# Kernel optimization log

Measured on AMD Instinct MI355X. Metric: run time of the kernel, lower is better.

Reference implementation:

```python
import jax, jax.numpy as jnp
import numpy as np
from jax import lax

B, T, F = 128, 100, 64
HID = [16, 32]  # encoder hidden dims; decoder uses reversed [32, 16]
K = 3


def _conv2d(x, w, b):
    # x: [N, Cin, H, W], w: [Cout, Cin, kh, kw] -> 'SAME' padding as in torch padding=k//2
    y = lax.conv_general_dilated(x, w, (1, 1), 'SAME',
                                 dimension_numbers=('NCHW', 'OIHW', 'NCHW'))
    return y + b[None, :, None, None]


def _convlstm_layer(xs, w, b, h0, c0):
    # xs: [T, B, Cin, H, W] time-major; returns hidden seq [T,B,Chid,H,W] and final (h, c)
    def step(carry, x_t):
        h, c = carry
        z = _conv2d(jnp.concatenate([x_t, h], axis=1), w, b)
        i, f, o, g = jnp.split(z, 4, axis=1)  # gate order i, f, o, g
        c2 = jax.nn.sigmoid(f) * c + jax.nn.sigmoid(i) * jnp.tanh(g)
        h2 = jax.nn.sigmoid(o) * jnp.tanh(c2)
        return (h2, c2), h2
    (hT, cT), hs = lax.scan(step, (h0, c0), xs)
    return hs, (hT, cT)


def setup_inputs() -> dict:
    key = jax.random.key(0)
    ks = jax.random.split(key, 12)
    s = 0.05
    inp = {
        'x': jax.random.normal(ks[0], (B, T, F), dtype=jnp.float32),
        # encoder layer 0: in=1+16, out=4*16
        'enc_w0': jax.random.normal(ks[1], (4 * HID[0], 1 + HID[0], K, K), dtype=jnp.float32) * s,
        'enc_b0': jnp.zeros((4 * HID[0],), dtype=jnp.float32),
        # encoder layer 1: in=16+32, out=4*32
        'enc_w1': jax.random.normal(ks[2], (4 * HID[1], HID[0] + HID[1], K, K), dtype=jnp.float32) * s,
        'enc_b1': jnp.zeros((4 * HID[1],), dtype=jnp.float32),
        # decoder layer 0: hidden=32, input=32 (last encoder hidden)
        'dec_w0': jax.random.normal(ks[3], (4 * HID[1], HID[1] + HID[1], K, K), dtype=jnp.float32) * s,
        'dec_b0': jnp.zeros((4 * HID[1],), dtype=jnp.float32),
        # decoder layer 1: hidden=16, input=32
        'dec_w1': jax.random.normal(ks[4], (4 * HID[0], HID[1] + HID[0], K, K), dtype=jnp.float32) * s,
        'dec_b1': jnp.zeros((4 * HID[0],), dtype=jnp.float32),
        # final 1x1 conv: 16 -> 1
        'fc_w': jax.random.normal(ks[5], (1, HID[0], 1, 1), dtype=jnp.float32) * s,
        'fc_b': jnp.zeros((1,), dtype=jnp.float32),
    }
    return inp


def reference(x, enc_w0, enc_b0, enc_w1, enc_b1, dec_w0, dec_b0, dec_w1, dec_b1, fc_w, fc_b):
    b, t, f = x.shape
    # [b,t,f] -> [t,b,1,f,1] time-major, spatial (f,1)
    xs = jnp.transpose(x.reshape(b, t, 1, f, 1), (1, 0, 2, 3, 4))
    z16 = jnp.zeros((b, HID[0], f, 1), x.dtype)
    z32 = jnp.zeros((b, HID[1], f, 1), x.dtype)

    enc1, (h1, c1) = _convlstm_layer(xs, enc_w0, enc_b0, z16, z16)
    enc2, (h2, c2) = _convlstm_layer(enc1, enc_w1, enc_b1, z32, z32)

    # decoder initial states = encoder final states reversed
    dec1, _ = _convlstm_layer(enc2, dec_w0, dec_b0, h2, c2)
    dec2, _ = _convlstm_layer(dec1, dec_w1, dec_b1, h1, c1)  # [t,b,16,f,1]

    # final 1x1 conv applied per timestep == one batched conv over t*b
    flat = dec2.reshape(t * b, HID[0], f, 1)
    out = _conv2d(flat, fc_w, fc_b)  # [t*b,1,f,1]
    recon = jnp.transpose(out.reshape(t, b, f), (1, 0, 2))  # [b,t,f]
    return recon
```

## Files before the change

kernel.cpp:

```cpp
#include <hip/hip_runtime.h>
#include <math.h>

#define B_ 128
#define T_ 100
#define RS 72
#define RS2 40

__device__ __forceinline__ float frcp_(float x){ return __builtin_amdgcn_rcpf(x); }
__device__ __forceinline__ float fsig_(float x){ return frcp_(1.f + __expf(-x)); }
__device__ __forceinline__ float ftanh_(float x){ float e = __expf(2.f*x); return 1.f - 2.f*frcp_(e+1.f); }
__device__ __forceinline__ float gate1(float zi, float zf, float zo, float zg, float& c){
    float cc = fsig_(zf)*c + fsig_(zi)*ftanh_(zg);
    c = cc;
    return fsig_(zo)*ftanh_(cc);
}
__device__ __forceinline__ float4 ldf4(const float* p){ return *reinterpret_cast<const float4*>(p); }
__device__ __forceinline__ void stf4(float* p, float4 v){ *reinterpret_cast<float4*>(p) = v; }
__device__ __forceinline__ float2 ldf2(const float* p){ return *reinterpret_cast<const float2*>(p); }
__device__ __forceinline__ void stf2(float* p, float2 v){ *reinterpret_cast<float2*>(p) = v; }
__device__ __forceinline__ float4 add4(float4 a, float4 b){
    return make_float4(a.x+b.x, a.y+b.y, a.z+b.z, a.w+b.w);
}
__device__ __forceinline__ float4 gate4(float4 zi, float4 zf, float4 zo, float4 zg,
                                        float bi, float bf, float bo, float bg, float4& c){
    float4 h;
    h.x = gate1(zi.x+bi, zf.x+bf, zo.x+bo, zg.x+bg, c.x);
    h.y = gate1(zi.y+bi, zf.y+bf, zo.y+bo, zg.y+bg, c.y);
    h.z = gate1(zi.z+bi, zf.z+bf, zo.z+bo, zg.z+bg, c.z);
    h.w = gate1(zi.w+bi, zf.w+bf, zo.w+bo, zg.w+bg, c.w);
    return h;
}

__device__ __forceinline__ void fma4v(float w, float u0,float u1,float u2,float u3, float4& a){
    a.x = fmaf(w,u0,a.x); a.y = fmaf(w,u1,a.y);
    a.z = fmaf(w,u2,a.z); a.w = fmaf(w,u3,a.w);
}
__device__ __forceinline__ void fma2v(float w, float u0,float u1, float2& a){
    a.x = fmaf(w,u0,a.x); a.y = fmaf(w,u1,a.y);
}

template<int ROWS>
__device__ __forceinline__ void rowacc4(const float* __restrict__ rowp,
                                        const float* __restrict__ wk,
                                        float4& ai, float4& af, float4& ao, float4& ag)
{
    float  m = rowp[-1];
    float4 a = ldf4(rowp);
    float  p = rowp[4];
    float4 wa = ldf4(wk);
    float4 wb = ldf4(wk + ROWS);
    float4 wc = ldf4(wk + 2*ROWS);
    fma4v(wa.x, m,a.x,a.y,a.z, ai);  fma4v(wa.y, m,a.x,a.y,a.z, af);
    fma4v(wa.z, m,a.x,a.y,a.z, ao);  fma4v(wa.w, m,a.x,a.y,a.z, ag);
    fma4v(wb.x, a.x,a.y,a.z,a.w, ai); fma4v(wb.y, a.x,a.y,a.z,a.w, af);
    fma4v(wb.z, a.x,a.y,a.z,a.w, ao); fma4v(wb.w, a.x,a.y,a.z,a.w, ag);
    fma4v(wc.x, a.y,a.z,a.w,p, ai);  fma4v(wc.y, a.y,a.z,a.w,p, af);
    fma4v(wc.z, a.y,a.z,a.w,p, ao);  fma4v(wc.w, a.y,a.z,a.w,p, ag);
}
template<int ROWS>
__device__ __forceinline__ void rowacc2(const float* __restrict__ rowp,
                                        const float* __restrict__ wk,
                                        float2& ai, float2& af, float2& ao, float2& ag)
{
    float  m = rowp[-1];
    float2 a = *reinterpret_cast<const float2*>(rowp);
    float  p = rowp[2];
    float4 wa = ldf4(wk);
    float4 wb = ldf4(wk + ROWS);
    float4 wc = ldf4(wk + 2*ROWS);
    fma2v(wa.x, m,a.x, ai); fma2v(wa.y, m,a.x, af);
    fma2v(wa.z, m,a.x, ao); fma2v(wa.w, m,a.x, ag);
    fma2v(wb.x, a.x,a.y, ai); fma2v(wb.y, a.x,a.y, af);
    fma2v(wb.z, a.x,a.y, ao); fma2v(wb.w, a.x,a.y, ag);
    fma2v(wc.x, a.y,p, ai); fma2v(wc.y, a.y,p, af);
    fma2v(wc.z, a.y,p, ao); fma2v(wc.w, a.y,p, ag);
}
template<int ROWS>
__device__ __forceinline__ void rowacc8(const float* __restrict__ rowp,
                                        const float* __restrict__ wk,
                                        float4& i0, float4& i1, float4& f0v, float4& f1v,
                                        float4& o0, float4& o1, float4& g0, float4& g1)
{
    float  m = rowp[-1];
    float4 a = ldf4(rowp);
    float4 b = ldf4(rowp + 4);
    float  p = rowp[8];
    float4 wa = ldf4(wk);
    float4 wb = ldf4(wk + ROWS);
    float4 wc = ldf4(wk + 2*ROWS);
    fma4v(wa.x, m,a.x,a.y,a.z, i0);   fma4v(wa.x, a.w,b.x,b.y,b.z, i1);
    fma4v(wa.y, m,a.x,a.y,a.z, f0v);  fma4v(wa.y, a.w,b.x,b.y,b.z, f1v);
    fma4v(wa.z, m,a.x,a.y,a.z, o0);   fma4v(wa.z, a.w,b.x,b.y,b.z, o1);
    fma4v(wa.w, m,a.x,a.y,a.z, g0);   fma4v(wa.w, a.w,b.x,b.y,b.z, g1);
    fma4v(wb.x, a.x,a.y,a.z,a.w, i0); fma4v(wb.x, b.x,b.y,b.z,b.w, i1);
    fma4v(wb.y, a.x,a.y,a.z,a.w, f0v);fma4v(wb.y, b.x,b.y,b.z,b.w, f1v);
    fma4v(wb.z, a.x,a.y,a.z,a.w, o0); fma4v(wb.z, b.x,b.y,b.z,b.w, o1);
    fma4v(wb.w, a.x,a.y,a.z,a.w, g0); fma4v(wb.w, b.x,b.y,b.z,b.w, g1);
    fma4v(wc.x, a.y,a.z,a.w,b.x, i0); fma4v(wc.x, b.y,b.z,b.w,p, i1);
    fma4v(wc.y, a.y,a.z,a.w,b.x, f0v);fma4v(wc.y, b.y,b.z,b.w,p, f1v);
    fma4v(wc.z, a.y,a.z,a.w,b.x, o0); fma4v(wc.z, b.y,b.z,b.w,p, o1);
    fma4v(wc.w, a.y,a.z,a.w,b.x, g0); fma4v(wc.w, b.y,b.z,b.w,p, g1);
}

__global__ __launch_bounds__(512, 1) void enc_kernel(
    const float* __restrict__ x,
    const float* __restrict__ w0, const float* __restrict__ b0,
    const float* __restrict__ w1, const float* __restrict__ b1,
    float* __restrict__ seq,
    float* __restrict__ h1f, float* __restrict__ c1f,
    float* __restrict__ h2f, float* __restrict__ c2f,
    float* __restrict__ comm, int* __restrict__ flags)
{
    __shared__ float wl0[51 * 64];
    __shared__ float wl1[144 * 128];
    __shared__ float bs0[64];
    __shared__ float bs1[128];
    __shared__ float hbuf[50 * RS2];
    __shared__ float zsA[4 * 16 * 32];
    __shared__ float zsB[4 * 32 * 32];

    const int tid = threadIdx.x;
    const int b = blockIdx.x & 127;
    const int s = blockIdx.x >> 7;
    const int gofs = s << 5;
    const int kg = tid >> 8;
    const int r  = tid & 255;
    const int chB = r >> 3, f0B = (r & 7) * 4;
    const int chA = r >> 4, f0A = (r & 15) * 2;
    const int haloSlot = s ? 3 : 36;
    const int myId = (b << 1) | s;
    const int peerId = myId ^ 1;
    float* mySend = &comm[(size_t)myId * 128];
    const float* peerBuf = &comm[(size_t)peerId * 128];

    for (int idx = tid; idx < 51 * 64; idx += 512) {
        int k = idx >> 6, rr = idx & 63;
        int ch = rr >> 2, g = rr & 3;
        int ci = k / 3, d = k - ci * 3;
        wl0[idx] = w0[((g * 16 + ch) * 17 + ci) * 9 + d * 3 + 1];
    }
    for (int idx = tid; idx < 144 * 128; idx += 512) {
        int k = idx >> 7, rr = idx & 127;
        int ch = rr >> 2, g = rr & 3;
        int ci = k / 3, d = k - ci * 3;
        wl1[idx] = w1[((g * 32 + ch) * 48 + ci) * 9 + d * 3 + 1];
    }
    if (tid < 64) bs0[tid] = b0[tid];
    if (tid < 128) bs1[tid] = b1[tid];
    for (int i = tid; i < 50 * RS2; i += 512) hbuf[i] = 0.f;
    __syncthreads();

    const int xl = tid - 256;
    if (xl >= 0 && xl < 34) {
        const int gc = gofs - 1 + xl;
        const bool v = (gc >= 0) && (gc < 64);
        hbuf[0 * RS2 + 3 + xl] = v ? x[(b * T_ + 0) * 64 + gc] : 0.f;
        hbuf[1 * RS2 + 3 + xl] = v ? x[(b * T_ + 1) * 64 + gc] : 0.f;
    }
    const float biA = bs0[chA], bfA = bs0[16+chA], boA = bs0[32+chA], bgA = bs0[48+chA];
    const float biB = bs1[chB], bfB = bs1[32+chB], boB = bs1[64+chB], bgB = bs1[96+chB];
    __syncthreads();

    const float4 z4 = make_float4(0.f, 0.f, 0.f, 0.f);
    const float2 z2 = make_float2(0.f, 0.f);
    float2 c0q = z2;
    float4 c1a = z4;

    if (kg == 0) {
        float2 ai = z2, af = z2, ao = z2, ag = z2;
        rowacc2<64>(&hbuf[0 * RS2 + 4 + f0A], &wl0[chA * 4], ai, af, ao, ag);
        float2 hq;
        hq.x = gate1(ai.x + biA, af.x + bfA, ao.x + boA, ag.x + bgA, c0q.x);
        hq.y = gate1(ai.y + biA, af.y + bfA, ao.y + boA, ag.y + bgA, c0q.y);
        *reinterpret_cast<float2*>(&hbuf[(2 + chA) * RS2 + 4 + f0A]) = hq;
        if ((r & 15) == (s ? 0 : 15)) {
            const float v = s ? hq.x : hq.y;
            __hip_atomic_store((unsigned int*)&mySend[1 * 64 + 32 + chA],
                               __float_as_uint(v),
                               __ATOMIC_RELAXED, __HIP_MEMORY_SCOPE_AGENT);
        }
    }
    __syncthreads();

#pragma unroll 1
    for (int t = 0; t < T_; ++t) {
        if (tid == 0)
            __hip_atomic_store(&flags[myId], t + 1,
                               __ATOMIC_RELAXED, __HIP_MEMORY_SCOPE_AGENT);
        if (tid < 48 && (t > 0 || tid >= 32)) {
            while (__hip_atomic_load(&flags[peerId],
                                     __ATOMIC_ACQUIRE, __HIP_MEMORY_SCOPE_AGENT) < t + 1)
                __builtin_amdgcn_s_sleep(2);
            const int par = (t + 1) & 1;
            const unsigned int uv =
                __hip_atomic_load((const unsigned int*)&peerBuf[par * 64 + tid],
                                  __ATOMIC_RELAXED, __HIP_MEMORY_SCOPE_AGENT);
            const float v = __uint_as_float(uv);
            if (tid < 32) hbuf[(18 + tid) * RS2 + haloSlot] = v;
            else          hbuf[(2 + (tid - 32)) * RS2 + haloSlot] = v;
        }
        __syncthreads();

        const bool doL0 = (t + 1 < T_);
        float4 I = z4, F = z4, O = z4, G = z4;
#pragma unroll 1
        for (int j = 0; j < 24; ++j) {
            const int ci = kg * 24 + j;
            rowacc4<128>(&hbuf[(2 + ci) * RS2 + 4 + f0B],
                         &wl1[(ci * 3) * 128 + chB * 4], I, F, O, G);
        }
        float2 ai = z2, af = z2, ao = z2, ag = z2;
        if (doL0) {
            if (kg == 0) {
                rowacc2<64>(&hbuf[((t + 1) & 1) * RS2 + 4 + f0A], &wl0[chA * 4],
                            ai, af, ao, ag);
#pragma unroll 1
                for (int j = 0; j < 8; ++j)
                    rowacc2<64>(&hbuf[(2 + j) * RS2 + 4 + f0A],
                                &wl0[((1 + j) * 3) * 64 + chA * 4], ai, af, ao, ag);
            } else {
#pragma unroll 1
                for (int j = 8; j < 16; ++j)
                    rowacc2<64>(&hbuf[(2 + j) * RS2 + 4 + f0A],
                                &wl0[((1 + j) * 3) * 64 + chA * 4], ai, af, ao, ag);
            }
        }
        if (kg == 1) {
            stf4(&zsB[(0*32+chB)*32 + f0B], I);
            stf4(&zsB[(1*32+chB)*32 + f0B], F);
            stf4(&zsB[(2*32+chB)*32 + f0B], O);
            stf4(&zsB[(3*32+chB)*32 + f0B], G);
            if (doL0) {
                *reinterpret_cast<float2*>(&zsA[(0*16+chA)*32 + f0A]) = ai;
                *reinterpret_cast<float2*>(&zsA[(1*16+chA)*32 + f0A]) = af;
                *reinterpret_cast<float2*>(&zsA[(2*16+chA)*32 + f0A]) = ao;
                *reinterpret_cast<float2*>(&zsA[(3*16+chA)*32 + f0A]) = ag;
            }
            if (xl >= 0 && xl < 34 && t + 2 < T_) {
                const int gc = gofs - 1 + xl;
                hbuf[(t & 1) * RS2 + 3 + xl] =
                    (gc >= 0 && gc < 64) ? x[(b * T_ + t + 2) * 64 + gc] : 0.f;
            }
        }
        __syncthreads();
        if (kg == 0) {
            float4 zi = add4(I, ldf4(&zsB[(0*32+chB)*32 + f0B]));
            float4 zf = add4(F, ldf4(&zsB[(1*32+chB)*32 + f0B]));
            float4 zo = add4(O, ldf4(&zsB[(2*32+chB)*32 + f0B]));
            float4 zg = add4(G, ldf4(&zsB[(3*32+chB)*32 + f0B]));
            float4 hq = gate4(zi, zf, zo, zg, biB, bfB, boB, bgB, c1a);
            stf4(&hbuf[(18 + chB) * RS2 + 4 + f0B], hq);
            stf4(&seq[((size_t)t * B_ + b) * 2048 + chB * 64 + gofs + f0B], hq);
            if (doL0 && (r & 7) == (s ? 0 : 7)) {
                const float v = s ? hq.x : hq.w;
                __hip_atomic_store((unsigned int*)&mySend[(t & 1) * 64 + chB],
                                   __float_as_uint(v),
                                   __ATOMIC_RELAXED, __HIP_MEMORY_SCOPE_AGENT);
            }
            if (doL0) {
                float2 pzi = *reinterpret_cast<const float2*>(&zsA[(0*16+chA)*32 + f0A]);
                float2 pzf = *reinterpret_cast<const float2*>(&zsA[(1*16+chA)*32 + f0A]);
                float2 pzo = *reinterpret_cast<const float2*>(&zsA[(2*16+chA)*32 + f0A]);
                float2 pzg = *reinterpret_cast<const float2*>(&zsA[(3*16+chA)*32 + f0A]);
                float2 hq2;
                hq2.x = gate1(ai.x+pzi.x+biA, af.x+pzf.x+bfA, ao.x+pzo.x+boA, ag.x+pzg.x+bgA, c0q.x);
                hq2.y = gate1(ai.y+pzi.y+biA, af.y+pzf.y+bfA, ao.y+pzo.y+boA, ag.y+pzg.y+bgA, c0q.y);
                *reinterpret_cast<float2*>(&hbuf[(2 + chA) * RS2 + 4 + f0A]) = hq2;
                if ((r & 15) == (s ? 0 : 15)) {
                    const float v = s ? hq2.x : hq2.y;
                    __hip_atomic_store((unsigned int*)&mySend[(t & 1) * 64 + 32 + chA],
                                       __float_as_uint(v),
                                       __ATOMIC_RELAXED, __HIP_MEMORY_SCOPE_AGENT);
                }
            }
        }
        __syncthreads();
    }

    if (kg == 0) {
        *reinterpret_cast<float2*>(&h1f[(b * 16 + chA) * 64 + gofs + f0A]) =
            *reinterpret_cast<const float2*>(&hbuf[(2 + chA) * RS2 + 4 + f0A]);
        *reinterpret_cast<float2*>(&c1f[(b * 16 + chA) * 64 + gofs + f0A]) = c0q;
        stf4(&h2f[b * 2048 + chB * 64 + gofs + f0B],
             ldf4(&hbuf[(18 + chB) * RS2 + 4 + f0B]));
        stf4(&c2f[b * 2048 + chB * 64 + gofs + f0B], c1a);
    }
}

__global__ __launch_bounds__(256, 2) void xconv0_kernel(
    const float* __restrict__ seqIn, const float* __restrict__ w,
    float* __restrict__ zx, int t0)
{
    __shared__ float wl[96 * 128];
    __shared__ float xt[32 * RS];

    const int tid = threadIdx.x;
    const int tl = blockIdx.x / B_;
    const int b  = blockIdx.x - tl * B_;
    const int t  = t0 + tl;

    for (int idx = tid; idx < 96 * 128; idx += 256) {
        int k = idx >> 7, rr = idx & 127;
        int ch = rr >> 2, g = rr & 3;
        int ci = k / 3, d = k - ci * 3;
        wl[idx] = w[((g * 32 + ch) * 64 + ci) * 9 + d * 3 + 1];
    }
    {
        int rr = tid >> 3, j = tid & 7;
        xt[rr * RS + (j < 4 ? j : 64 + j)] = 0.f;
    }
    {
        const float* s = &seqIn[((size_t)t * B_ + b) * 2048 + tid * 8];
        float4 v0 = ldf4(s);
        float4 v1 = ldf4(s + 4);
        int ci = tid >> 3, col = (tid & 7) * 8;
        stf4(&xt[ci * RS + 4 + col], v0);
        stf4(&xt[ci * RS + 4 + col + 4], v1);
    }
    __syncthreads();

    const int ch = tid >> 3, f0 = (tid & 7) * 8;
    const float4 z4 = make_float4(0.f,0.f,0.f,0.f);
    float4 i0=z4,i1=z4,f0v=z4,f1v=z4,o0=z4,o1=z4,g0=z4,g1=z4;
#pragma unroll 1
    for (int rr = 0; rr < 32; ++rr)
        rowacc8<128>(&xt[rr * RS + 4 + f0], wl + (rr * 3) * 128 + ch * 4,
                     i0, i1, f0v, f1v, o0, o1, g0, g1);

    float* zp = &zx[(((size_t)tl * B_ + b) * 4) * 2048 + ch * 64 + f0];
    stf4(zp, i0);            stf4(zp + 4, i1);
    stf4(zp + 2048, f0v);    stf4(zp + 2048 + 4, f1v);
    stf4(zp + 4096, o0);     stf4(zp + 4096 + 4, o1);
    stf4(zp + 6144, g0);     stf4(zp + 6144 + 4, g1);
}

__global__ __launch_bounds__(512, 1) void decg(
    const float* __restrict__ w0, const float* __restrict__ b0,
    const float* __restrict__ w1, const float* __restrict__ b1,
    const float* __restrict__ zx,
    const float* __restrict__ h0in, const float* __restrict__ c0in,
    const float* __restrict__ h1in, const float* __restrict__ c1in,
    float* __restrict__ h0sv, float* __restrict__ c0sv,
    float* __restrict__ h1sv, float* __restrict__ c1sv,
    const float* __restrict__ fw, const float* __restrict__ fb,
    float* __restrict__ out,
    float* __restrict__ comm0, float* __restrict__ comm1,
    int* __restrict__ flg, int t0, int tn, int lastc)
{
    __shared__ float wl0[96 * 128];
    __shared__ float wl1[144 * 64];
    __shared__ float hp0[32 * RS2];
    __shared__ float hp1[16 * RS2];
    __shared__ float zs0[4 * 32 * 32];
    __shared__ float zs1[4 * 16 * 32];
    __shared__ float bs0[128];
    __shared__ float bs1[64];
    __shared__ float fcw[16];
    __shared__ float fcb_s;

    const int tid = threadIdx.x;
    const int b = blockIdx.x & 127;
    const int s = blockIdx.x >> 7;
    const int gofs = s << 5;
    const int haloSlot = s ? 3 : 36;
    const int bcol = s ? 31 : 32;
    const int myId = (b << 1) | s, peerId = myId ^ 1;
    float* send0 = &comm0[(size_t)myId * 64];
    const float* peer0 = &comm0[(size_t)peerId * 64];
    float* send1 = &comm1[(size_t)myId * 32];
    const float* peer1 = &comm1[(size_t)peerId * 32];

    const int kg = tid >> 8;
    const int r = tid & 255;
    const bool isD0 = (r < 128);
    const int ch0 = r >> 2, t0f = (r & 3) * 8;
    const int r1 = r - 128;
    const int ch1 = r1 >> 3, t1f = (r1 & 7) * 4;

    for (int idx = tid; idx < 96 * 128; idx += 512) {
        int k = idx >> 7, rr = idx & 127;
        int c8 = rr >> 2, g = rr & 3;
        int ci = k / 3, d = k - ci * 3;
        wl0[idx] = w0[((g * 32 + c8) * 64 + 32 + ci) * 9 + d * 3 + 1];
    }
    for (int idx = tid; idx < 144 * 64; idx += 512) {
        int k = idx >> 6, rr = idx & 63;
        int c8 = rr >> 2, g = rr & 3;
        int ci = k / 3, d = k - ci * 3;
        wl1[idx] = w1[((g * 16 + c8) * 48 + ci) * 9 + d * 3 + 1];
    }
    if (tid < 128) bs0[tid] = b0[tid];
    if (tid < 64) bs1[tid] = b1[tid];
    if (tid < 16) fcw[tid] = fw[tid];
    if (tid == 16) fcb_s = fb[0];
    for (int i = tid; i < 32 * RS2; i += 512) hp0[i] = 0.f;
    for (int i = tid; i < 16 * RS2; i += 512) hp1[i] = 0.f;
    __syncthreads();

    for (int i = tid; i < 1024; i += 512) {
        int c8 = i >> 5, f = i & 31;
        hp0[c8 * RS2 + 4 + f] = h0in[b * 2048 + c8 * 64 + gofs + f];
    }
    { int c8 = tid >> 5, f = tid & 31;
      hp1[c8 * RS2 + 4 + f] = h1in[b * 1024 + c8 * 64 + gofs + f]; }
    if (tid < 32) hp0[tid * RS2 + haloSlot] = h0in[b * 2048 + tid * 64 + bcol];
    if (tid >= 64 && tid < 80)
        hp1[(tid - 64) * RS2 + haloSlot] = h1in[b * 1024 + (tid - 64) * 64 + bcol];

    const float4 z4 = make_float4(0.f, 0.f, 0.f, 0.f);
    float4 c0a = z4, c0b = z4;
    float4 c1v = z4;
    float bi, bfv, bo, bg;
    if (isD0) { bi = bs0[ch0]; bfv = bs0[32+ch0]; bo = bs0[64+ch0]; bg = bs0[96+ch0]; }
    else      { bi = bs1[ch1]; bfv = bs1[16+ch1]; bo = bs1[32+ch1]; bg = bs1[48+ch1]; }
    if (kg == 0) {
        if (isD0) {
            c0a = ldf4(&c0in[b * 2048 + ch0 * 64 + gofs + t0f]);
            c0b = ldf4(&c0in[b * 2048 + ch0 * 64 + gofs + t0f + 4]);
        } else {
            c1v = ldf4(&c1in[b * 1024 + ch1 * 64 + gofs + t1f]);
        }
    }
    const float fcbv = fcb_s;

#pragma unroll 1
    for (int u = t0; u < t0 + tn + lastc; ++u) {
        if (tid == 0)
            __hip_atomic_store(&flg[myId], u,
                               __ATOMIC_RELAXED, __HIP_MEMORY_SCOPE_AGENT);
        if (u > t0) {
            const int par = (u - 1) & 1;
            if (tid < 32) {
                while (__hip_atomic_load(&flg[peerId],
                                         __ATOMIC_ACQUIRE, __HIP_MEMORY_SCOPE_AGENT) < u)
                    __builtin_amdgcn_s_sleep(2);
                hp0[tid * RS2 + haloSlot] = __uint_as_float(
                    __hip_atomic_load((const unsigned int*)&peer0[par * 32 + tid],
                                      __ATOMIC_RELAXED, __HIP_MEMORY_SCOPE_AGENT));
            } else if (tid >= 64 && tid < 80 && u >= 2) {
                while (__hip_atomic_load(&flg[peerId],
                                         __ATOMIC_ACQUIRE, __HIP_MEMORY_SCOPE_AGENT) < u)
                    __builtin_amdgcn_s_sleep(2);
                hp1[(tid - 64) * RS2 + haloSlot] = __uint_as_float(
                    __hip_atomic_load((const unsigned int*)&peer1[par * 16 + (tid - 64)],
                                      __ATOMIC_RELAXED, __HIP_MEMORY_SCOPE_AGENT));
            }
        }
        __syncthreads();

        const bool d0act = (u - t0 < tn);
        const bool d1act = (u >= 1);
        float4 A0=z4,A1=z4,B0=z4,B1=z4,C0=z4,C1=z4,D0=z4,D1=z4;
        float4 ai=z4, af=z4, ao=z4, ag=z4;
        float4 X0=z4,X1=z4,X2=z4,X3=z4,X4=z4,X5=z4,X6=z4,X7=z4;

        if (isD0) {
            if (d0act) {
                if (kg == 0) {
                    const float* zp = &zx[(((size_t)(u - t0) * B_ + b) * 4) * 2048
                                          + ch0 * 64 + gofs + t0f];
                    X0 = ldf4(zp);         X1 = ldf4(zp + 4);
                    X2 = ldf4(zp + 2048);  X3 = ldf4(zp + 2052);
                    X4 = ldf4(zp + 4096);  X5 = ldf4(zp + 4100);
                    X6 = ldf4(zp + 6144);  X7 = ldf4(zp + 6148);
                }
#pragma unroll 1
                for (int j = 0; j < 16; ++j) {
                    const int ci = kg * 16 + j;
                    rowacc8<128>(&hp0[ci * RS2 + 4 + t0f], &wl0[(ci * 3) * 128 + ch0 * 4],
                                 A0, A1, B0, B1, C0, C1, D0, D1);
                }
            }
            if (kg == 1 && r < 32 && u >= 2) {
                float a = fcbv;
#pragma unroll
                for (int k2 = 0; k2 < 16; ++k2)
                    a = fmaf(fcw[k2], hp1[k2 * RS2 + 4 + r], a);
                out[(b * T_ + (u - 2)) * 64 + gofs + r] = a;
            }
        } else if (d1act) {
            if (kg == 0) {
#pragma unroll 1
                for (int j = 0; j < 24; ++j)
                    rowacc4<64>(&hp0[j * RS2 + 4 + t1f], &wl1[(j * 3) * 64 + ch1 * 4],
                                ai, af, ao, ag);
            } else {
#pragma unroll 1
                for (int j = 24; j < 32; ++j)
                    rowacc4<64>(&hp0[j * RS2 + 4 + t1f], &wl1[(j * 3) * 64 + ch1 * 4],
                                ai, af, ao, ag);
#pragma unroll 1
                for (int j = 0; j < 16; ++j)
                    rowacc4<64>(&hp1[j * RS2 + 4 + t1f], &wl1[((32 + j) * 3) * 64 + ch1 * 4],
                                ai, af, ao, ag);
            }
        }
        if (kg == 1) {
            if (isD0) { if (d0act) {
                stf4(&zs0[(0*32+ch0)*32 + t0f], A0); stf4(&zs0[(0*32+ch0)*32 + t0f + 4], A1);
                stf4(&zs0[(1*32+ch0)*32 + t0f], B0); stf4(&zs0[(1*32+ch0)*32 + t0f + 4], B1);
                stf4(&zs0[(2*32+ch0)*32 + t0f], C0); stf4(&zs0[(2*32+ch0)*32 + t0f + 4], C1);
                stf4(&zs0[(3*32+ch0)*32 + t0f], D0); stf4(&zs0[(3*32+ch0)*32 + t0f + 4], D1);
            }} else { if (d1act) {
                stf4(&zs1[(0*16+ch1)*32 + t1f], ai);
                stf4(&zs1[(1*16+ch1)*32 + t1f], af);
                stf4(&zs1[(2*16+ch1)*32 + t1f], ao);
                stf4(&zs1[(3*16+ch1)*32 + t1f], ag);
            }}
        }
        __syncthreads();
        if (kg == 0) {
            if (isD0 && d0act) {
                float4 zi0 = add4(add4(A0, X0), ldf4(&zs0[(0*32+ch0)*32 + t0f]));
                float4 zi1 = add4(add4(A1, X1), ldf4(&zs0[(0*32+ch0)*32 + t0f + 4]));
                float4 zf0 = add4(add4(B0, X2), ldf4(&zs0[(1*32+ch0)*32 + t0f]));
                float4 zf1 = add4(add4(B1, X3), ldf4(&zs0[(1*32+ch0)*32 + t0f + 4]));
                float4 zo0 = add4(add4(C0, X4), ldf4(&zs0[(2*32+ch0)*32 + t0f]));
                float4 zo1 = add4(add4(C1, X5), ldf4(&zs0[(2*32+ch0)*32 + t0f + 4]));
                float4 zg0 = add4(add4(D0, X6), ldf4(&zs0[(3*32+ch0)*32 + t0f]));
                float4 zg1 = add4(add4(D1, X7), ldf4(&zs0[(3*32+ch0)*32 + t0f + 4]));
                float4 h0q0 = gate4(zi0, zf0, zo0, zg0, bi, bfv, bo, bg, c0a);
                float4 h0q1 = gate4(zi1, zf1, zo1, zg1, bi, bfv, bo, bg, c0b);
                stf4(&hp0[ch0 * RS2 + 4 + t0f], h0q0);
                stf4(&hp0[ch0 * RS2 + 4 + t0f + 4], h0q1);
                if ((r & 3) == (s ? 0 : 3)) {
                    __hip_atomic_store((unsigned int*)&send0[(u & 1) * 32 + ch0],
                                       __float_as_uint(s ? h0q0.x : h0q1.w),
                                       __ATOMIC_RELAXED, __HIP_MEMORY_SCOPE_AGENT);
                }
            } else if (!isD0 && d1act) {
                float4 zi = add4(ai, ldf4(&zs1[(0*16+ch1)*32 + t1f]));
                float4 zf = add4(af, ldf4(&zs1[(1*16+ch1)*32 + t1f]));
                float4 zo = add4(ao, ldf4(&zs1[(2*16+ch1)*32 + t1f]));
                float4 zg = add4(ag, ldf4(&zs1[(3*16+ch1)*32 + t1f]));
                float4 h1q = gate4(zi, zf, zo, zg, bi, bfv, bo, bg, c1v);
                stf4(&hp1[ch1 * RS2 + 4 + t1f], h1q);
                if ((r1 & 7) == (s ? 0 : 7)) {
                    __hip_atomic_store((unsigned int*)&send1[(u & 1) * 16 + ch1],
                                       __float_as_uint(s ? h1q.x : h1q.w),
                                       __ATOMIC_RELAXED, __HIP_MEMORY_SCOPE_AGENT);
                }
            }
        }
        __syncthreads();
    }

    if (lastc && tid < 32) {
        float a = fcbv;
#pragma unroll
        for (int k2 = 0; k2 < 16; ++k2)
            a = fmaf(fcw[k2], hp1[k2 * RS2 + 4 + tid], a);
        out[(b * T_ + (T_ - 1)) * 64 + gofs + tid] = a;
    }
    for (int i = tid; i < 1024; i += 512) {
        int c8 = i >> 5, f = i & 31;
        h0sv[b * 2048 + c8 * 64 + gofs + f] = hp0[c8 * RS2 + 4 + f];
    }
    { int c8 = tid >> 5, f = tid & 31;
      h1sv[b * 1024 + c8 * 64 + gofs + f] = hp1[c8 * RS2 + 4 + f]; }
    if (kg == 0) {
        if (isD0) {
            stf4(&c0sv[b * 2048 + ch0 * 64 + gofs + t0f], c0a);
            stf4(&c0sv[b * 2048 + ch0 * 64 + gofs + t0f + 4], c0b);
        } else {
            stf4(&c1sv[b * 1024 + ch1 * 64 + gofs + t1f], c1v);
        }
    }
}

__global__ __launch_bounds__(512, 1) void dec0_fb(
    const float* __restrict__ w, const float* __restrict__ bias,
    float* __restrict__ seq,
    const float* __restrict__ hin, const float* __restrict__ cin)
{
    __shared__ float wl[192 * 128];
    __shared__ float bs[128];
    __shared__ float xin[32 * RS];
    __shared__ float hp[32 * RS];

    const int tid = threadIdx.x;
    const int b = blockIdx.x;

    for (int idx = tid; idx < 192 * 128; idx += 512) {
        int k = idx >> 7, rr = idx & 127;
        int ch = rr >> 2, g = rr & 3;
        int ci = k / 3, d = k - ci * 3;
        wl[idx] = w[((g * 32 + ch) * 64 + ci) * 9 + d * 3 + 1];
    }
    if (tid < 128) bs[tid] = bias[tid];
    for (int i = tid; i < 32 * RS; i += 512) { xin[i] = 0.f; hp[i] = 0.f; }
    __syncthreads();
    {
        const float* hs = &hin[b * 2048 + tid * 4];
        float4 hv = ldf4(hs);
        int ci = tid >> 4, col = (tid & 15) * 4;
        stf4(&hp[ci * RS + 4 + col], hv);
    }
    const int ch = tid >> 4, f0 = (tid & 15) * 4;
    float4 cc = ldf4(&cin[b * 2048 + ch * 64 + f0]);
    const float bi = bs[ch], bf = bs[32 + ch], bo = bs[64 + ch], bg = bs[96 + ch];
    const float4 z4 = make_float4(0.f,0.f,0.f,0.f);

    float4 nx = ldf4(&seq[(size_t)b * 2048 + tid * 4]);

#pragma unroll 1
    for (int t = 0; t < T_; ++t) {
        {
            int ci = tid >> 4, col = (tid & 15) * 4;
            stf4(&xin[ci * RS + 4 + col], nx);
        }
        __syncthreads();
        if (t + 1 < T_)
            nx = ldf4(&seq[((size_t)(t + 1) * B_ + b) * 2048 + tid * 4]);
        float4 ai = z4, af = z4, ao = z4, ag = z4;
#pragma unroll 1
        for (int rr = 0; rr < 32; ++rr)
            rowacc4<128>(&xin[rr * RS + 4 + f0], wl + (rr * 3) * 128 + ch * 4, ai, af, ao, ag);
#pragma unroll 1
        for (int rr = 0; rr < 32; ++rr)
            rowacc4<128>(&hp[rr * RS + 4 + f0], wl + ((32 + rr) * 3) * 128 + ch * 4, ai, af, ao, ag);
        float4 hn = gate4(ai, af, ao, ag, bi, bf, bo, bg, cc);
        __syncthreads();
        stf4(&hp[ch * RS + 4 + f0], hn);
        stf4(&seq[((size_t)t * B_ + b) * 2048 + ch * 64 + f0], hn);
    }
}

__global__ __launch_bounds__(512, 1) void dec1_fb(
    const float* __restrict__ w, const float* __restrict__ bias,
    const float* __restrict__ seq,
    const float* __restrict__ hin, const float* __restrict__ cin,
    const float* __restrict__ fw, const float* __restrict__ fb,
    float* __restrict__ out)
{
    __shared__ float wl[144 * 64];
    __shared__ float bs[64];
    __shared__ float xin[32 * RS];
    __shared__ float hp[16 * RS];
    __shared__ float fcw[16];
    __shared__ float fcb;

    const int tid = threadIdx.x;
    const int b = blockIdx.x;

    for (int idx = tid; idx < 144 * 64; idx += 512) {
        int k = idx >> 6, rr = idx & 63;
        int ch = rr >> 2, g = rr & 3;
        int ci = k / 3, d = k - ci * 3;
        wl[idx] = w[((g * 16 + ch) * 48 + ci) * 9 + d * 3 + 1];
    }
    if (tid < 64) bs[tid] = bias[tid];
    if (tid < 16) fcw[tid] = fw[tid];
    if (tid == 16) fcb = fb[0];
    for (int i = tid; i < 32 * RS; i += 512) xin[i] = 0.f;
    for (int i = tid; i < 16 * RS; i += 512) hp[i] = 0.f;
    __syncthreads();
    {
        const float* hs = &hin[b * 1024 + tid * 2];
        float2 hv = *reinterpret_cast<const float2*>(hs);
        int ci = tid >> 5, col = (tid & 31) * 2;
        *reinterpret_cast<float2*>(&hp[ci * RS + 4 + col]) = hv;
    }
    const int ch = tid >> 5, f0 = (tid & 31) * 2;
    float2 cc = *reinterpret_cast<const float2*>(&cin[b * 1024 + ch * 64 + f0]);
    const float bi = bs[ch], bf = bs[16 + ch], bo = bs[32 + ch], bg = bs[48 + ch];
    const float2 z2 = make_float2(0.f,0.f);
    float4 nx = ldf4(&seq[(size_t)b * 2048 + tid * 4]);
    __syncthreads();

#pragma unroll 1
    for (int t = 0; t < T_; ++t) {
        {
            int ci = tid >> 4, col = (tid & 15) * 4;
            stf4(&xin[ci * RS + 4 + col], nx);
        }
        __syncthreads();
        if (t + 1 < T_)
            nx = ldf4(&seq[((size_t)(t + 1) * B_ + b) * 2048 + tid * 4]);

        float2 ai = z2, af = z2, ao = z2, ag = z2;
#pragma unroll 1
        for (int rr = 0; rr < 32; ++rr)
            rowacc2<64>(&xin[rr * RS + 4 + f0], wl + (rr * 3) * 64 + ch * 4, ai, af, ao, ag);
#pragma unroll 1
        for (int rr = 0; rr < 16; ++rr)
            rowacc2<64>(&hp[rr * RS + 4 + f0], wl + ((32 + rr) * 3) * 64 + ch * 4, ai, af, ao, ag);

        float2 hh;
        hh.x = gate1(ai.x + bi, af.x + bf, ao.x + bo, ag.x + bg, cc.x);
        hh.y = gate1(ai.y + bi, af.y + bf, ao.y + bo, ag.y + bg, cc.y);
        __syncthreads();
        *reinterpret_cast<float2*>(&hp[ch * RS + 4 + f0]) = hh;
        __syncthreads();

        if (tid < 64) {
            float a = fcb;
#pragma unroll
            for (int k2 = 0; k2 < 16; ++k2)
                a = fmaf(fcw[k2], hp[k2 * RS + 4 + tid], a);
            out[(b * T_ + t) * 64 + tid] = a;
        }
    }
}

extern "C" void kernel_launch(void* const* d_in, const int* in_sizes, int n_in,
                              void* d_out, int out_size, void* d_ws, size_t ws_size,
                              hipStream_t stream)
{
    (void)in_sizes; (void)n_in; (void)out_size;
    const float* x   = (const float*)d_in[0];
    const float* ew0 = (const float*)d_in[1];
    const float* eb0 = (const float*)d_in[2];
    const float* ew1 = (const float*)d_in[3];
    const float* eb1 = (const float*)d_in[4];
    const float* dw0 = (const float*)d_in[5];
    const float* db0 = (const float*)d_in[6];
    const float* dw1 = (const float*)d_in[7];
    const float* db1 = (const float*)d_in[8];
    const float* fw  = (const float*)d_in[9];
    const float* fb  = (const float*)d_in[10];
    float* out = (float*)d_out;

    float* ws  = (float*)d_ws;
    size_t off = 0;
    float* seq = ws + off; off += (size_t)T_ * B_ * 2048;
    float* h1f = ws + off; off += (size_t)B_ * 1024;
    float* c1f = ws + off; off += (size_t)B_ * 1024;
    float* h2f = ws + off; off += (size_t)B_ * 2048;
    float* c2f = ws + off; off += (size_t)B_ * 2048;
    float* hd0 = ws + off; off += (size_t)B_ * 2048;
    float* cd0 = ws + off; off += (size_t)B_ * 2048;
    float* hd1 = ws + off; off += (size_t)B_ * 1024;
    float* cd1 = ws + off; off += (size_t)B_ * 1024;
    float* comm = ws + off; off += 32768 + 16384 + 8192;
    int*   flg  = (int*)(ws + off); off += 1024;
    float* zx  = ws + off;

    float* commD0 = comm + 32768;
    float* commD1 = comm + 32768 + 16384;

    size_t availf = (ws_size / 4 > off) ? (ws_size / 4 - off) : 0;
    int TC = 0;
    if      (availf >= (size_t)100 * B_ * 8192) TC = 100;
    else if (availf >= (size_t)50  * B_ * 8192) TC = 50;
    else if (availf >= (size_t)25  * B_ * 8192) TC = 25;
    else if (availf >= (size_t)10  * B_ * 8192) TC = 10;

    hipMemsetAsync(flg, 0, 512 * sizeof(int), stream);
    enc_kernel<<<256, 512, 0, stream>>>(x, ew0, eb0, ew1, eb1, seq,
                                        h1f, c1f, h2f, c2f, comm, flg);

    if (TC > 0) {
        for (int t0 = 0; t0 < T_; t0 += TC) {
            int tn = (t0 + TC <= T_) ? TC : (T_ - t0);
            int lastc = (t0 + tn >= T_) ? 1 : 0;
            xconv0_kernel<<<tn * B_, 256, 0, stream>>>(seq, dw0, zx, t0);
            decg<<<256, 512, 0, stream>>>(
                dw0, db0, dw1, db1, zx,
                t0 == 0 ? h2f : hd0, t0 == 0 ? c2f : cd0,
                t0 == 0 ? h1f : hd1, t0 == 0 ? c1f : cd1,
                hd0, cd0, hd1, cd1,
                fw, fb, out, commD0, commD1, flg + 256, t0, tn, lastc);
        }
    } else {
        dec0_fb<<<B_, 512, 0, stream>>>(dw0, db0, seq, h2f, c2f);
        dec1_fb<<<B_, 512, 0, stream>>>(dw1, db1, seq, h1f, c1f, fw, fb, out);
    }
}
```

Measured before the change: 2.066 ms.

## Split encoder reduction across four thread groups with 1024-thread blocks

The encoder kernel moves from 512 to 1024 threads per block, so the layer-1 input-channel reduction is split four ways (12 channels each) instead of two. Partial sums from three groups go to a larger shared buffer and group 0 combines them. Layer-0 work moves to groups 2 and 3, and the gate stage runs alongside the layer-1 gates. The zs shared layouts in encoder and decoder change to a linear per-thread stride so accesses are contiguous. The aim is to shorten the per-timestep serial critical path, at the cost of more shared memory, a larger cross-group reduction and register pressure from the 1024-thread launch bound.

New measurement: 2.008 ms. -2.8%, faster.

```diff
diff --git a/kernel.cpp b/kernel.cpp
--- a/kernel.cpp
+++ b/kernel.cpp
@@ -102,7 +102,7 @@
     fma4v(wc.w, a.y,a.z,a.w,b.x, g0); fma4v(wc.w, b.y,b.z,b.w,p, g1);
 }
 
-__global__ __launch_bounds__(512, 1) void enc_kernel(
+__global__ __launch_bounds__(1024, 4) void enc_kernel(
     const float* __restrict__ x,
     const float* __restrict__ w0, const float* __restrict__ b0,
     const float* __restrict__ w1, const float* __restrict__ b1,
@@ -116,14 +116,14 @@
     __shared__ float bs0[64];
     __shared__ float bs1[128];
     __shared__ float hbuf[50 * RS2];
-    __shared__ float zsA[4 * 16 * 32];
-    __shared__ float zsB[4 * 32 * 32];
+    __shared__ float zsA[2048];
+    __shared__ float zsB3[3 * 4096];
 
     const int tid = threadIdx.x;
     const int b = blockIdx.x & 127;
     const int s = blockIdx.x >> 7;
     const int gofs = s << 5;
-    const int kg = tid >> 8;
+    const int g  = tid >> 8;
     const int r  = tid & 255;
     const int chB = r >> 3, f0B = (r & 7) * 4;
     const int chA = r >> 4, f0A = (r & 15) * 2;
@@ -133,21 +133,21 @@
     float* mySend = &comm[(size_t)myId * 128];
     const float* peerBuf = &comm[(size_t)peerId * 128];
 
-    for (int idx = tid; idx < 51 * 64; idx += 512) {
+    for (int idx = tid; idx < 51 * 64; idx += 1024) {
         int k = idx >> 6, rr = idx & 63;
-        int ch = rr >> 2, g = rr & 3;
+        int ch = rr >> 2, gg = rr & 3;
         int ci = k / 3, d = k - ci * 3;
-        wl0[idx] = w0[((g * 16 + ch) * 17 + ci) * 9 + d * 3 + 1];
-    }
-    for (int idx = tid; idx < 144 * 128; idx += 512) {
+        wl0[idx] = w0[((gg * 16 + ch) * 17 + ci) * 9 + d * 3 + 1];
+    }
+    for (int idx = tid; idx < 144 * 128; idx += 1024) {
         int k = idx >> 7, rr = idx & 127;
-        int ch = rr >> 2, g = rr & 3;
+        int ch = rr >> 2, gg = rr & 3;
         int ci = k / 3, d = k - ci * 3;
-        wl1[idx] = w1[((g * 32 + ch) * 48 + ci) * 9 + d * 3 + 1];
+        wl1[idx] = w1[((gg * 32 + ch) * 48 + ci) * 9 + d * 3 + 1];
     }
     if (tid < 64) bs0[tid] = b0[tid];
     if (tid < 128) bs1[tid] = b1[tid];
-    for (int i = tid; i < 50 * RS2; i += 512) hbuf[i] = 0.f;
+    for (int i = tid; i < 50 * RS2; i += 1024) hbuf[i] = 0.f;
     __syncthreads();
 
     const int xl = tid - 256;
@@ -166,7 +166,7 @@
     float2 c0q = z2;
     float4 c1a = z4;
 
-    if (kg == 0) {
+    if (g == 2) {
         float2 ai = z2, af = z2, ao = z2, ag = z2;
         rowacc2<64>(&hbuf[0 * RS2 + 4 + f0A], &wl0[chA * 4], ai, af, ao, ag);
         float2 hq;
@@ -204,50 +204,49 @@
         const bool doL0 = (t + 1 < T_);
         float4 I = z4, F = z4, O = z4, G = z4;
 #pragma unroll 1
-        for (int j = 0; j < 24; ++j) {
-            const int ci = kg * 24 + j;
+        for (int j = 0; j < 12; ++j) {
+            const int ci = 12 * g + j;
             rowacc4<128>(&hbuf[(2 + ci) * RS2 + 4 + f0B],
                          &wl1[(ci * 3) * 128 + chB * 4], I, F, O, G);
         }
         float2 ai = z2, af = z2, ao = z2, ag = z2;
         if (doL0) {
-            if (kg == 0) {
+            if (g == 2) {
                 rowacc2<64>(&hbuf[((t + 1) & 1) * RS2 + 4 + f0A], &wl0[chA * 4],
                             ai, af, ao, ag);
 #pragma unroll 1
                 for (int j = 0; j < 8; ++j)
                     rowacc2<64>(&hbuf[(2 + j) * RS2 + 4 + f0A],
                                 &wl0[((1 + j) * 3) * 64 + chA * 4], ai, af, ao, ag);
-            } else {
+            } else if (g == 3) {
 #pragma unroll 1
                 for (int j = 8; j < 16; ++j)
                     rowacc2<64>(&hbuf[(2 + j) * RS2 + 4 + f0A],
                                 &wl0[((1 + j) * 3) * 64 + chA * 4], ai, af, ao, ag);
             }
         }
-        if (kg == 1) {
-            stf4(&zsB[(0*32+chB)*32 + f0B], I);
-            stf4(&zsB[(1*32+chB)*32 + f0B], F);
-            stf4(&zsB[(2*32+chB)*32 + f0B], O);
-            stf4(&zsB[(3*32+chB)*32 + f0B], G);
-            if (doL0) {
-                *reinterpret_cast<float2*>(&zsA[(0*16+chA)*32 + f0A]) = ai;
-                *reinterpret_cast<float2*>(&zsA[(1*16+chA)*32 + f0A]) = af;
-                *reinterpret_cast<float2*>(&zsA[(2*16+chA)*32 + f0A]) = ao;
-                *reinterpret_cast<float2*>(&zsA[(3*16+chA)*32 + f0A]) = ag;
-            }
-            if (xl >= 0 && xl < 34 && t + 2 < T_) {
-                const int gc = gofs - 1 + xl;
-                hbuf[(t & 1) * RS2 + 3 + xl] =
-                    (gc >= 0 && gc < 64) ? x[(b * T_ + t + 2) * 64 + gc] : 0.f;
-            }
-        }
-        __syncthreads();
-        if (kg == 0) {
-            float4 zi = add4(I, ldf4(&zsB[(0*32+chB)*32 + f0B]));
-            float4 zf = add4(F, ldf4(&zsB[(1*32+chB)*32 + f0B]));
-            float4 zo = add4(O, ldf4(&zsB[(2*32+chB)*32 + f0B]));
-            float4 zg = add4(G, ldf4(&zsB[(3*32+chB)*32 + f0B]));
+        if (g != 0) {
+            float* zp = &zsB3[(g - 1) * 4096 + r * 4];
+            stf4(zp, I); stf4(zp + 1024, F); stf4(zp + 2048, O); stf4(zp + 3072, G);
+        }
+        if (g == 3 && doL0) {
+            float* zp = &zsA[r * 2];
+            stf2(zp, ai); stf2(zp + 512, af); stf2(zp + 1024, ao); stf2(zp + 1536, ag);
+        }
+        if (xl >= 0 && xl < 34 && t + 2 < T_) {
+            const int gc = gofs - 1 + xl;
+            hbuf[(t & 1) * RS2 + 3 + xl] =
+                (gc >= 0 && gc < 64) ? x[(b * T_ + t + 2) * 64 + gc] : 0.f;
+        }
+        __syncthreads();
+        if (g == 0) {
+            const float* p0 = &zsB3[0 * 4096 + r * 4];
+            const float* p1 = &zsB3[1 * 4096 + r * 4];
+            const float* p2 = &zsB3[2 * 4096 + r * 4];
+            float4 zi = add4(add4(I, ldf4(p0)),        add4(ldf4(p1),        ldf4(p2)));
+            float4 zf = add4(add4(F, ldf4(p0 + 1024)), add4(ldf4(p1 + 1024), ldf4(p2 + 1024)));
+            float4 zo = add4(add4(O, ldf4(p0 + 2048)), add4(ldf4(p1 + 2048), ldf4(p2 + 2048)));
+            float4 zg = add4(add4(G, ldf4(p0 + 3072)), add4(ldf4(p1 + 3072), ldf4(p2 + 3072)));
             float4 hq = gate4(zi, zf, zo, zg, biB, bfB, boB, bgB, c1a);
             stf4(&hbuf[(18 + chB) * RS2 + 4 + f0B], hq);
             stf4(&seq[((size_t)t * B_ + b) * 2048 + chB * 64 + gofs + f0B], hq);
@@ -257,30 +256,32 @@
                                    __float_as_uint(v),
                                    __ATOMIC_RELAXED, __HIP_MEMORY_SCOPE_AGENT);
             }
-            if (doL0) {
-                float2 pzi = *reinterpret_cast<const float2*>(&zsA[(0*16+chA)*32 + f0A]);
-                float2 pzf = *reinterpret_cast<const float2*>(&zsA[(1*16+chA)*32 + f0A]);
-                float2 pzo = *reinterpret_cast<const float2*>(&zsA[(2*16+chA)*32 + f0A]);
-                float2 pzg = *reinterpret_cast<const float2*>(&zsA[(3*16+chA)*32 + f0A]);
-                float2 hq2;
-                hq2.x = gate1(ai.x+pzi.x+biA, af.x+pzf.x+bfA, ao.x+pzo.x+boA, ag.x+pzg.x+bgA, c0q.x);
-                hq2.y = gate1(ai.y+pzi.y+biA, af.y+pzf.y+bfA, ao.y+pzo.y+boA, ag.y+pzg.y+bgA, c0q.y);
-                *reinterpret_cast<float2*>(&hbuf[(2 + chA) * RS2 + 4 + f0A]) = hq2;
-                if ((r & 15) == (s ? 0 : 15)) {
-                    const float v = s ? hq2.x : hq2.y;
-                    __hip_atomic_store((unsigned int*)&mySend[(t & 1) * 64 + 32 + chA],
-                                       __float_as_uint(v),
-                                       __ATOMIC_RELAXED, __HIP_MEMORY_SCOPE_AGENT);
-                }
+        }
+        if (g == 2 && doL0) {
+            float2 pzi = ldf2(&zsA[r * 2]);
+            float2 pzf = ldf2(&zsA[512 + r * 2]);
+            float2 pzo = ldf2(&zsA[1024 + r * 2]);
+            float2 pzg = ldf2(&zsA[1536 + r * 2]);
+            float2 hq2;
+            hq2.x = gate1(ai.x+pzi.x+biA, af.x+pzf.x+bfA, ao.x+pzo.x+boA, ag.x+pzg.x+bgA, c0q.x);
+            hq2.y = gate1(ai.y+pzi.y+biA, af.y+pzf.y+bfA, ao.y+pzo.y+boA, ag.y+pzg.y+bgA, c0q.y);
+            *reinterpret_cast<float2*>(&hbuf[(2 + chA) * RS2 + 4 + f0A]) = hq2;
+            if ((r & 15) == (s ? 0 : 15)) {
+                const float v = s ? hq2.x : hq2.y;
+                __hip_atomic_store((unsigned int*)&mySend[(t & 1) * 64 + 32 + chA],
+                                   __float_as_uint(v),
+                                   __ATOMIC_RELAXED, __HIP_MEMORY_SCOPE_AGENT);
             }
         }
         __syncthreads();
     }
 
-    if (kg == 0) {
+    if (g == 2) {
         *reinterpret_cast<float2*>(&h1f[(b * 16 + chA) * 64 + gofs + f0A]) =
             *reinterpret_cast<const float2*>(&hbuf[(2 + chA) * RS2 + 4 + f0A]);
         *reinterpret_cast<float2*>(&c1f[(b * 16 + chA) * 64 + gofs + f0A]) = c0q;
+    }
+    if (g == 0) {
         stf4(&h2f[b * 2048 + chB * 64 + gofs + f0B],
              ldf4(&hbuf[(18 + chB) * RS2 + 4 + f0B]));
         stf4(&c2f[b * 2048 + chB * 64 + gofs + f0B], c1a);
@@ -351,7 +352,7 @@
     __shared__ float wl1[144 * 64];
     __shared__ float hp0[32 * RS2];
     __shared__ float hp1[16 * RS2];
-    __shared__ float zs0[4 * 32 * 32];
+    __shared__ float zs0[4096];
     __shared__ float zs1[4 * 16 * 32];
     __shared__ float bs0[128];
     __shared__ float bs1[64];
@@ -497,10 +498,11 @@
         }
         if (kg == 1) {
             if (isD0) { if (d0act) {
-                stf4(&zs0[(0*32+ch0)*32 + t0f], A0); stf4(&zs0[(0*32+ch0)*32 + t0f + 4], A1);
-                stf4(&zs0[(1*32+ch0)*32 + t0f], B0); stf4(&zs0[(1*32+ch0)*32 + t0f + 4], B1);
-                stf4(&zs0[(2*32+ch0)*32 + t0f], C0); stf4(&zs0[(2*32+ch0)*32 + t0f + 4], C1);
-                stf4(&zs0[(3*32+ch0)*32 + t0f], D0); stf4(&zs0[(3*32+ch0)*32 + t0f + 4], D1);
+                float* zp = &zs0[r * 4];
+                stf4(zp + 0,    A0); stf4(zp + 512,  A1);
+                stf4(zp + 1024, B0); stf4(zp + 1536, B1);
+                stf4(zp + 2048, C0); stf4(zp + 2560, C1);
+                stf4(zp + 3072, D0); stf4(zp + 3584, D1);
             }} else { if (d1act) {
                 stf4(&zs1[(0*16+ch1)*32 + t1f], ai);
                 stf4(&zs1[(1*16+ch1)*32 + t1f], af);
@@ -511,14 +513,15 @@
         __syncthreads();
         if (kg == 0) {
             if (isD0 && d0act) {
-                float4 zi0 = add4(add4(A0, X0), ldf4(&zs0[(0*32+ch0)*32 + t0f]));
-                float4 zi1 = add4(add4(A1, X1), ldf4(&zs0[(0*32+ch0)*32 + t0f + 4]));
-                float4 zf0 = add4(add4(B0, X2), ldf4(&zs0[(1*32+ch0)*32 + t0f]));
-                float4 zf1 = add4(add4(B1, X3), ldf4(&zs0[(1*32+ch0)*32 + t0f + 4]));
-                float4 zo0 = add4(add4(C0, X4), ldf4(&zs0[(2*32+ch0)*32 + t0f]));
-                float4 zo1 = add4(add4(C1, X5), ldf4(&zs0[(2*32+ch0)*32 + t0f + 4]));
-                float4 zg0 = add4(add4(D0, X6), ldf4(&zs0[(3*32+ch0)*32 + t0f]));
-                float4 zg1 = add4(add4(D1, X7), ldf4(&zs0[(3*32+ch0)*32 + t0f + 4]));
+                const float* zp = &zs0[r * 4];
+                float4 zi0 = add4(add4(A0, X0), ldf4(zp));
+                float4 zi1 = add4(add4(A1, X1), ldf4(zp + 512));
+                float4 zf0 = add4(add4(B0, X2), ldf4(zp + 1024));
+                float4 zf1 = add4(add4(B1, X3), ldf4(zp + 1536));
+                float4 zo0 = add4(add4(C0, X4), ldf4(zp + 2048));
+                float4 zo1 = add4(add4(C1, X5), ldf4(zp + 2560));
+                float4 zg0 = add4(add4(D0, X6), ldf4(zp + 3072));
+                float4 zg1 = add4(add4(D1, X7), ldf4(zp + 3584));
                 float4 h0q0 = gate4(zi0, zf0, zo0, zg0, bi, bfv, bo, bg, c0a);
                 float4 h0q1 = gate4(zi1, zf1, zo1, zg1, bi, bfv, bo, bg, c0b);
                 stf4(&hp0[ch0 * RS2 + 4 + t0f], h0q0);
@@ -747,8 +750,8 @@
     else if (availf >= (size_t)10  * B_ * 8192) TC = 10;
 
     hipMemsetAsync(flg, 0, 512 * sizeof(int), stream);
-    enc_kernel<<<256, 512, 0, stream>>>(x, ew0, eb0, ew1, eb1, seq,
-                                        h1f, c1f, h2f, c2f, comm, flg);
+    enc_kernel<<<256, 1024, 0, stream>>>(x, ew0, eb0, ew1, eb1, seq,
+                                         h1f, c1f, h2f, c2f, comm, flg);
 
     if (TC > 0) {
         for (int t0 = 0; t0 < T_; t0 += TC) {
```
